# Kernel optimization log

Measured on AMD Instinct MI355X. Metric: run time of the kernel, lower is better.

The kernel has to match this reference:

```python
import jax, jax.numpy as jnp
import numpy as np

N_NODES = 50000
N_EDGES = 150000
N_GRAPHS = 1024
IN_DIM = 78
OUT_DIM = 64
HEADS = 10
HID = OUT_DIM * HEADS  # 640
NEG_SLOPE = 0.2


def _add_self_loops(edge_index, num_nodes):
    loop = jnp.arange(num_nodes, dtype=edge_index.dtype)
    src = jnp.concatenate([edge_index[0], loop])
    dst = jnp.concatenate([edge_index[1], loop])
    return src, dst


def gatv2_conv(x, edge_index, Wl, Wr, att, bias, heads, out_dim):
    # PyG GATv2Conv (share_weights=False, concat=True, add_self_loops=True),
    # inference mode so attention dropout is a no-op.
    N = x.shape[0]
    src, dst = _add_self_loops(edge_index, N)
    xl = (x @ Wl).reshape(N, heads, out_dim)  # source transform
    xr = (x @ Wr).reshape(N, heads, out_dim)  # target transform
    s = jax.nn.leaky_relu(xl[src] + xr[dst], NEG_SLOPE)      # [E,H,C]
    logits = jnp.einsum('ehc,hc->eh', s, att)                # [E,H]
    m = jax.ops.segment_max(logits, dst, num_segments=N)     # [N,H] (self-loops => no empty segs)
    ex = jnp.exp(logits - m[dst])
    den = jax.ops.segment_sum(ex, dst, num_segments=N)
    alpha = ex / den[dst]                                    # scatter-softmax over in-edges
    out = jax.ops.segment_sum(alpha[:, :, None] * xl[src], dst, num_segments=N)
    return out.reshape(N, heads * out_dim) + bias


def gcn_conv(x, edge_index, W, b):
    N = x.shape[0]
    src, dst = _add_self_loops(edge_index, N)
    deg = jax.ops.segment_sum(jnp.ones(src.shape[0], x.dtype), dst, num_segments=N)
    dinv = jax.lax.rsqrt(jnp.maximum(deg, 1.0))
    norm = dinv[src] * dinv[dst]                             # [E]
    xw = x @ W
    return jax.ops.segment_sum(norm[:, None] * xw[src], dst, num_segments=N) + b


def setup_inputs() -> dict:
    key = jax.random.key(0)
    ks = jax.random.split(key, 16)
    x = jax.random.normal(ks[0], (N_NODES, IN_DIM), dtype=jnp.float32)
    edge_index = jax.random.randint(ks[1], (2, N_EDGES), 0, N_NODES, dtype=jnp.int64)
    batch = jnp.sort(jax.random.randint(ks[2], (N_NODES,), 0, N_GRAPHS, dtype=jnp.int64))

    def glorot(k, shape, fan_in):
        return jax.random.normal(k, shape, dtype=jnp.float32) * (1.0 / np.sqrt(fan_in))

    return {
        'x': x, 'edge_index': edge_index, 'batch': batch,
        'Wl1': glorot(ks[3], (IN_DIM, HID), IN_DIM),
        'Wr1': glorot(ks[4], (IN_DIM, HID), IN_DIM),
        'a1': glorot(ks[5], (HEADS, OUT_DIM), OUT_DIM),
        'b1': jnp.zeros((HID,), jnp.float32),
        'Wl2': glorot(ks[6], (HID, HID), HID),
        'Wr2': glorot(ks[7], (HID, HID), HID),
        'a2': glorot(ks[8], (1, HID), HID),
        'b2': jnp.zeros((HID,), jnp.float32),
        'Wg': glorot(ks[9], (HID, HID), HID),
        'bg': jnp.zeros((HID,), jnp.float32),
    }


def reference(x, edge_index, batch, Wl1, Wr1, a1, b1, Wl2, Wr2, a2, b2, Wg, bg):
    # inference: feature dropout layers are identity
    h = jax.nn.elu(gatv2_conv(x, edge_index, Wl1, Wr1, a1, b1, HEADS, OUT_DIM))
    h = gatv2_conv(h, edge_index, Wl2, Wr2, a2, b2, 1, HID)
    h = gcn_conv(h, edge_index, Wg, bg)
    h = jax.nn.relu(h)
    # global max pool + global mean pool per graph
    gmax = jax.ops.segment_max(h, batch, num_segments=N_GRAPHS)
    cnt = jax.ops.segment_sum(jnp.ones((h.shape[0],), h.dtype), batch, num_segments=N_GRAPHS)
    gmean = jax.ops.segment_sum(h, batch, num_segments=N_GRAPHS) / jnp.maximum(cnt, 1.0)[:, None]
    return jnp.concatenate([gmax, gmean], axis=1)
```

## Files before the change

### kernel.cpp

```cpp
#include <hip/hip_runtime.h>
#include <hip/hip_bf16.h>
#include <cstdint>
#include <cstddef>

typedef __hip_bfloat16 bf16;

#define N_NODES  50000
#define N_EDGES  150000
#define N_GRAPHS 1024
#define IN_DIM   78
#define K1P      128
#define OUT_DIM  64
#define HEADS    10
#define HID      640
#define NEG_SLOPE 0.2f
#define SCB      ((N_NODES + 255) / 256)

static __device__ __forceinline__ float b2f(bf16 v){ return __bfloat162float(v); }
static __device__ __forceinline__ bf16  f2b(float v){ return __float2bfloat16(v); }

__device__ __forceinline__ int clampi(int v, int hi){ return v < 0 ? 0 : (v >= hi ? hi - 1 : v); }

__device__ __forceinline__ float bf2f_bits(short s){
  return __uint_as_float(((unsigned)(unsigned short)s) << 16);
}
__device__ __forceinline__ short f2bf_bits(float v){
  unsigned u = __float_as_uint(v);
  return (short)((u + 0x7fffu + ((u >> 16) & 1u)) >> 16);
}

__global__ __launch_bounds__(256) void fill_u32(unsigned* __restrict__ p, unsigned v, int n){
  int i = blockIdx.x * 256 + threadIdx.x;
  if (i < n) p[i] = v;
}

__global__ __launch_bounds__(256) void conv_x(const float* __restrict__ x, bf16* __restrict__ XB){
  int i = blockIdx.x * 256 + threadIdx.x;
  if (i >= N_NODES * K1P) return;
  int n = i / K1P, k = i - n * K1P;
  XB[i] = f2b(k < IN_DIM ? x[(size_t)n * IN_DIM + k] : 0.f);
}

__global__ __launch_bounds__(256) void conv_wT2(const float* __restrict__ W0,
                                                const float* __restrict__ W1,
                                                bf16* __restrict__ WT,
                                                int K, int N, int Kp){
  int i = blockIdx.x * 256 + threadIdx.x;
  const int per = N * Kp;
  if (i >= 2 * per) return;
  int m = i / per, r = i - m * per;
  const float* W = m == 0 ? W0 : W1;
  int n = r / Kp, k = r - n * Kp;
  WT[i] = f2b(k < K ? W[(size_t)k * N + n] : 0.f);
}

__global__ __launch_bounds__(256) void conv_wT3t(const float* __restrict__ W0,
                                                 const float* __restrict__ W1,
                                                 const float* __restrict__ W2,
                                                 bf16* __restrict__ WT){
  __shared__ float t[32][33];
  int m = blockIdx.z;
  const float* W = m == 0 ? W0 : (m == 1 ? W1 : W2);
  int n0 = blockIdx.x * 32, k0 = blockIdx.y * 32;
  int tx = threadIdx.x & 31, ty = threadIdx.x >> 5;
#pragma unroll
  for (int r = 0; r < 32; r += 8)
    t[ty + r][tx] = W[(size_t)(k0 + ty + r) * HID + n0 + tx];
  __syncthreads();
  bf16* O = WT + (size_t)m * HID * HID;
#pragma unroll
  for (int r = 0; r < 32; r += 8)
    O[(size_t)(n0 + ty + r) * HID + k0 + tx] = f2b(t[tx][ty + r]);
}

#define BM 128
#define BN 128
#define BK 64

typedef __attribute__((ext_vector_type(8))) short bf16x8;
typedef __attribute__((ext_vector_type(4))) float f32x4;

typedef const __attribute__((address_space(1))) unsigned gu32;
typedef __attribute__((address_space(3))) unsigned lu32;

__global__ __launch_bounds__(256) void mfma_gemm(const bf16* __restrict__ A,
                                                 const bf16* __restrict__ BT,
                                                 bf16* __restrict__ C0,
                                                 bf16* __restrict__ C1,
                                                 int M, int Kp, int NB){
  int d   = blockIdx.x;
  int xcd = d & 7, j = d >> 3;
  int cb  = j % NB, ri = j / NB;
  int rb  = ri * 8 + xcd;
  const int row0 = rb * BM;
  if (row0 >= M) return;
  const int col0 = cb * BN;

  __shared__ short As[BM * BK];
  __shared__ short Bs[BN * BK];
  const int tid  = threadIdx.x;
  const int lane = tid & 63;
  const int wave = tid >> 6;
  const int wr   = (wave >> 1) * 64;
  const int wc   = (wave & 1) * 64;
  const int l15  = lane & 15;
  const int quad = lane >> 4;
  const int sw   = l15 & 7;

  const bf16* aptr[4];
  const bf16* bptr[4];
  lu32* lda[4];
  lu32* ldb[4];
#pragma unroll
  for (int t = 0; t < 4; ++t){
    int ci = (t * 4 + wave) * 64 + lane;
    int r  = ci >> 3;
    int sc = (ci & 7) ^ (r & 7);
    int gr = row0 + r; if (gr >= M) gr = M - 1;
    aptr[t] = A  + (size_t)gr * Kp + sc * 8;
    bptr[t] = BT + (size_t)(col0 + r) * Kp + sc * 8;
    lda[t]  = (lu32*)(&As[(t * 4 + wave) * 512]);
    ldb[t]  = (lu32*)(&Bs[(t * 4 + wave) * 512]);
  }

  f32x4 acc[4][4];
#pragma unroll
  for (int i = 0; i < 4; ++i)
#pragma unroll
    for (int jj = 0; jj < 4; ++jj) acc[i][jj] = (f32x4){0.f, 0.f, 0.f, 0.f};

  for (int k0 = 0; k0 < Kp; k0 += BK){
#pragma unroll
    for (int t = 0; t < 4; ++t){
      __builtin_amdgcn_global_load_lds((gu32*)(aptr[t] + k0), lda[t], 16, 0, 0);
      __builtin_amdgcn_global_load_lds((gu32*)(bptr[t] + k0), ldb[t], 16, 0, 0);
    }
    __syncthreads();

#pragma unroll
    for (int ks = 0; ks < 2; ++ks){
      const int slotA = ((ks * 4 + quad) ^ sw) * 8;
      bf16x8 af[4], bfr[4];
#pragma unroll
      for (int i = 0; i < 4; ++i)
        af[i] = *(bf16x8*)(&As[(wr + i * 16 + l15) * BK + slotA]);
#pragma unroll
      for (int jj = 0; jj < 4; ++jj)
        bfr[jj] = *(bf16x8*)(&Bs[(wc + jj * 16 + l15) * BK + slotA]);
#pragma unroll
      for (int i = 0; i < 4; ++i)
#pragma unroll
        for (int jj = 0; jj < 4; ++jj)
          acc[i][jj] = __builtin_amdgcn_mfma_f32_16x16x32_bf16(af[i], bfr[jj], acc[i][jj], 0, 0, 0);
    }
    __syncthreads();
  }

  if (row0 + BM <= M){
#pragma unroll
    for (int i = 0; i < 4; ++i){
#pragma unroll
      for (int jj = 0; jj < 4; ++jj){
        int gc = col0 + wc + jj * 16 + l15;
        bf16* Cp = (gc < HID) ? C0 : C1;
        size_t cc = (gc < HID) ? gc : gc - HID;
        size_t base = (size_t)(row0 + wr + i * 16 + quad * 4) * HID + cc;
#pragma unroll
        for (int r = 0; r < 4; ++r)
          Cp[base + (size_t)r * HID] = f2b(acc[i][jj][r]);
      }
    }
  } else {
#pragma unroll
    for (int i = 0; i < 4; ++i){
#pragma unroll
      for (int jj = 0; jj < 4; ++jj){
        int gc = col0 + wc + jj * 16 + l15;
        bf16* Cp = (gc < HID) ? C0 : C1;
        int cc   = (gc < HID) ? gc : gc - HID;
#pragma unroll
        for (int r = 0; r < 4; ++r){
          int gr = row0 + wr + i * 16 + quad * 4 + r;
          if (gr < M) Cp[(size_t)gr * HID + cc] = f2b(acc[i][jj][r]);
        }
      }
    }
  }
}

__global__ __launch_bounds__(256) void count_deg(const int* __restrict__ edst, int* __restrict__ degi){
  int e = blockIdx.x * 256 + threadIdx.x;
  if (e >= N_EDGES) return;
  atomicAdd(&degi[clampi(edst[e], N_NODES)], 1);
}

__global__ __launch_bounds__(256) void scan_blk(const int* __restrict__ degi,
                                                int* __restrict__ rowp,
                                                float* __restrict__ dinv,
                                                int* __restrict__ bsum){
  __shared__ int wsum[4];
  int b = blockIdx.x, tid = threadIdx.x;
  int i = b * 256 + tid;
  int lane = tid & 63, wv = tid >> 6;
  int v = (i < N_NODES) ? degi[i] : 0;
  int incl = v;
#pragma unroll
  for (int ofs = 1; ofs < 64; ofs <<= 1){
    int t = __shfl_up(incl, ofs);
    if (lane >= ofs) incl += t;
  }
  if (lane == 63) wsum[wv] = incl;
  __syncthreads();
  int woff = 0;
#pragma unroll
  for (int w = 0; w < 4; ++w) if (w < wv) woff += wsum[w];
  if (i < N_NODES){
    rowp[i] = woff + incl - v;
    dinv[i] = rsqrtf((float)(v + 1));
  }
  if (tid == 0) bsum[b] = wsum[0] + wsum[1] + wsum[2] + wsum[3];
}

__global__ __launch_bounds__(256) void scan_top(int* __restrict__ bsum, int* __restrict__ rowp){
  __shared__ int wsum[4];
  int tid = threadIdx.x, lane = tid & 63, wv = tid >> 6;
  int v = (tid < SCB) ? bsum[tid] : 0;
  int incl = v;
#pragma unroll
  for (int ofs = 1; ofs < 64; ofs <<= 1){
    int t = __shfl_up(incl, ofs);
    if (lane >= ofs) incl += t;
  }
  if (lane == 63) wsum[wv] = incl;
  __syncthreads();
  int woff = 0;
#pragma unroll
  for (int w = 0; w < 4; ++w) if (w < wv) woff += wsum[w];
  if (tid < SCB) bsum[tid] = woff + incl - v;
  if (tid == 255) rowp[N_NODES] = woff + incl;
}

__global__ __launch_bounds__(256) void scan_add(const int* __restrict__ bsum,
                                                int* __restrict__ rowp,
                                                int* __restrict__ curs){
  int i = blockIdx.x * 256 + threadIdx.x;
  if (i >= N_NODES) return;
  int r = rowp[i] + bsum[blockIdx.x];
  rowp[i] = r; curs[i] = r;
}

__global__ __launch_bounds__(256) void bucket_edges(const int* __restrict__ esrc,
                                                    const int* __restrict__ edst,
                                                    int* __restrict__ curs,
                                                    int* __restrict__ srcg,
                                                    int* __restrict__ dstg){
  int e = blockIdx.x * 256 + threadIdx.x;
  if (e >= N_EDGES) return;
  int d = clampi(edst[e], N_NODES);
  int pos = atomicAdd(&curs[d], 1);
  srcg[pos] = clampi(esrc[e], N_NODES);
  dstg[pos] = d;
}

__global__ __launch_bounds__(256) void gat1_fused(const bf16* __restrict__ xl,
                                                  const bf16* __restrict__ xr,
                                                  const int* __restrict__ srcg,
                                                  const int* __restrict__ rowp,
                                                  const float* __restrict__ att,
                                                  const float* __restrict__ bias,
                                                  bf16* __restrict__ H){
  int n    = (blockIdx.x * 256 + threadIdx.x) >> 6;
  int lane = threadIdx.x & 63;
  if (n >= N_NODES) return;
  int r0 = rowp[n], r1 = rowp[n + 1];

  float4 aA0 = *(const float4*)(att + 8 * lane);
  float4 aA1 = *(const float4*)(att + 8 * lane + 4);
  float2 aBv = *(const float2*)(att + 512 + 2 * lane);
  float attA[8] = {aA0.x, aA0.y, aA0.z, aA0.w, aA1.x, aA1.y, aA1.z, aA1.w};
  float attB0 = aBv.x, attB1 = aBv.y;

  const bf16* xrn = xr + (size_t)n * HID;
  bf16x8 vr = *(const bf16x8*)(xrn + 8 * lane);
  unsigned ur = *(const unsigned*)(xrn + 512 + 2 * lane);
  float xrA[8];
#pragma unroll
  for (int j = 0; j < 8; ++j) xrA[j] = bf2f_bits(vr[j]);
  float xrB0 = bf2f_bits((short)(ur & 0xffff));
  float xrB1 = bf2f_bits((short)(ur >> 16));

  auto logits = [&](const float* xA, float xB0, float xB1, float& lA, float& lB){
    float pa = 0.f;
#pragma unroll
    for (int j = 0; j < 8; ++j){
      float s = xA[j] + xrA[j];
      s *= (s > 0.f) ? 1.f : NEG_SLOPE;
      pa = fmaf(attA[j], s, pa);
    }
    pa += __shfl_xor(pa, 1);
    pa += __shfl_xor(pa, 2);
    pa += __shfl_xor(pa, 4);
    lA = pa;
    float s0 = xB0 + xrB0; s0 *= (s0 > 0.f) ? 1.f : NEG_SLOPE;
    float s1 = xB1 + xrB1; s1 *= (s1 > 0.f) ? 1.f : NEG_SLOPE;
    float pb = attB0 * s0 + attB1 * s1;
    pb += __shfl_xor(pb, 1);
    pb += __shfl_xor(pb, 2);
    pb += __shfl_xor(pb, 4);
    pb += __shfl_xor(pb, 8);
    pb += __shfl_xor(pb, 16);
    lB = pb;
  };

  const bf16* xn = xl + (size_t)n * HID;
  bf16x8 v0 = *(const bf16x8*)(xn + 8 * lane);
  unsigned u0 = *(const unsigned*)(xn + 512 + 2 * lane);
  float accA[8];
  float sA[8];
#pragma unroll
  for (int j = 0; j < 8; ++j){ sA[j] = bf2f_bits(v0[j]); accA[j] = sA[j]; }
  float sB0 = bf2f_bits((short)(u0 & 0xffff));
  float sB1 = bf2f_bits((short)(u0 >> 16));
  float accB0 = sB0, accB1 = sB1;
  float mA, mB;
  logits(sA, sB0, sB1, mA, mB);
  float denA = 1.f, denB = 1.f;

  int p = r0;
  for (; p + 1 < r1; p += 2){
    int s0i = srcg[p], s1i = srcg[p + 1];
    const bf16* q0 = xl + (size_t)s0i * HID;
    const bf16* q1 = xl + (size_t)s1i * HID;
    bf16x8 w0 = *(const bf16x8*)(q0 + 8 * lane);
    unsigned t0 = *(const unsigned*)(q0 + 512 + 2 * lane);
    bf16x8 w1 = *(const bf16x8*)(q1 + 8 * lane);
    unsigned t1 = *(const unsigned*)(q1 + 512 + 2 * lane);
    float yA0[8], yA1[8];
#pragma unroll
    for (int j = 0; j < 8; ++j){ yA0[j] = bf2f_bits(w0[j]); yA1[j] = bf2f_bits(w1[j]); }
    float yB00 = bf2f_bits((short)(t0 & 0xffff)), yB01 = bf2f_bits((short)(t0 >> 16));
    float yB10 = bf2f_bits((short)(t1 & 0xffff)), yB11 = bf2f_bits((short)(t1 >> 16));
    float lA0, lB0, lA1, lB1;
    logits(yA0, yB00, yB01, lA0, lB0);
    logits(yA1, yB10, yB11, lA1, lB1);
    {
      float m2 = fmaxf(mA, fmaxf(lA0, lA1));
      float sc = __expf(mA - m2);
      float p0 = __expf(lA0 - m2), p1 = __expf(lA1 - m2);
      denA = denA * sc + p0 + p1; mA = m2;
#pragma unroll
      for (int j = 0; j < 8; ++j) accA[j] = accA[j] * sc + p0 * yA0[j] + p1 * yA1[j];
    }
    {
      float m2 = fmaxf(mB, fmaxf(lB0, lB1));
      float sc = __expf(mB - m2);
      float p0 = __expf(lB0 - m2), p1 = __expf(lB1 - m2);
      denB = denB * sc + p0 + p1; mB = m2;
      accB0 = accB0 * sc + p0 * yB00 + p1 * yB10;
      accB1 = accB1 * sc + p0 * yB01 + p1 * yB11;
    }
  }
  if (p < r1){
    int si = srcg[p];
    const bf16* q0 = xl + (size_t)si * HID;
    bf16x8 w0 = *(const bf16x8*)(q0 + 8 * lane);
    unsigned t0 = *(const unsigned*)(q0 + 512 + 2 * lane);
    float yA0[8];
#pragma unroll
    for (int j = 0; j < 8; ++j) yA0[j] = bf2f_bits(w0[j]);
    float yB00 = bf2f_bits((short)(t0 & 0xffff)), yB01 = bf2f_bits((short)(t0 >> 16));
    float lA0, lB0;
    logits(yA0, yB00, yB01, lA0, lB0);
    {
      float m2 = fmaxf(mA, lA0);
      float sc = __expf(mA - m2);
      float p0 = __expf(lA0 - m2);
      denA = denA * sc + p0; mA = m2;
#pragma unroll
      for (int j = 0; j < 8; ++j) accA[j] = accA[j] * sc + p0 * yA0[j];
    }
    {
      float m2 = fmaxf(mB, lB0);
      float sc = __expf(mB - m2);
      float p0 = __expf(lB0 - m2);
      denB = denB * sc + p0; mB = m2;
      accB0 = accB0 * sc + p0 * yB00;
      accB1 = accB1 * sc + p0 * yB01;
    }
  }

  float invA = 1.f / denA, invB = 1.f / denB;
  float4 bA0 = *(const float4*)(bias + 8 * lane);
  float4 bA1 = *(const float4*)(bias + 8 * lane + 4);
  float2 bB  = *(const float2*)(bias + 512 + 2 * lane);
  float bAa[8] = {bA0.x, bA0.y, bA0.z, bA0.w, bA1.x, bA1.y, bA1.z, bA1.w};
  bf16x8 oA;
#pragma unroll
  for (int j = 0; j < 8; ++j){
    float v = accA[j] * invA + bAa[j];
    v = v > 0.f ? v : (__expf(v) - 1.f);
    oA[j] = f2bf_bits(v);
  }
  float vb0 = accB0 * invB + bB.x; vb0 = vb0 > 0.f ? vb0 : (__expf(vb0) - 1.f);
  float vb1 = accB1 * invB + bB.y; vb1 = vb1 > 0.f ? vb1 : (__expf(vb1) - 1.f);
  bf16* hn = H + (size_t)n * HID;
  *(bf16x8*)(hn + 8 * lane) = oA;
  unsigned ob = (unsigned)(unsigned short)f2bf_bits(vb0) |
                ((unsigned)(unsigned short)f2bf_bits(vb1) << 16);
  *(unsigned*)(hn + 512 + 2 * lane) = ob;
}

__global__ __launch_bounds__(256) void gat2_fused(const bf16* __restrict__ xl,
                                                  const bf16* __restrict__ xr,
                                                  const int* __restrict__ srcg,
                                                  const int* __restrict__ rowp,
                                                  const float* __restrict__ att,
                                                  const float* __restrict__ bias,
                                                  bf16* __restrict__ H){
  int n    = (blockIdx.x * 256 + threadIdx.x) >> 6;
  int lane = threadIdx.x & 63;
  if (n >= N_NODES) return;
  int r0 = rowp[n], r1 = rowp[n + 1];

  float4 aA0 = *(const float4*)(att + 8 * lane);
  float4 aA1 = *(const float4*)(att + 8 * lane + 4);
  float2 aBv = *(const float2*)(att + 512 + 2 * lane);
  float attA[8] = {aA0.x, aA0.y, aA0.z, aA0.w, aA1.x, aA1.y, aA1.z, aA1.w};
  float attB0 = aBv.x, attB1 = aBv.y;

  const bf16* xrn = xr + (size_t)n * HID;
  bf16x8 vr = *(const bf16x8*)(xrn + 8 * lane);
  unsigned ur = *(const unsigned*)(xrn + 512 + 2 * lane);
  float xrA[8];
#pragma unroll
  for (int j = 0; j < 8; ++j) xrA[j] = bf2f_bits(vr[j]);
  float xrB0 = bf2f_bits((short)(ur & 0xffff));
  float xrB1 = bf2f_bits((short)(ur >> 16));

  auto logit1 = [&](const float* xA, float xB0, float xB1)->float{
    float s0 = xB0 + xrB0; s0 *= (s0 > 0.f) ? 1.f : NEG_SLOPE;
    float s1 = xB1 + xrB1; s1 *= (s1 > 0.f) ? 1.f : NEG_SLOPE;
    float pa = attB0 * s0 + attB1 * s1;
#pragma unroll
    for (int j = 0; j < 8; ++j){
      float s = xA[j] + xrA[j];
      s *= (s > 0.f) ? 1.f : NEG_SLOPE;
      pa = fmaf(attA[j], s, pa);
    }
    pa += __shfl_xor(pa, 1);
    pa += __shfl_xor(pa, 2);
    pa += __shfl_xor(pa, 4);
    pa += __shfl_xor(pa, 8);
    pa += __shfl_xor(pa, 16);
    pa += __shfl_xor(pa, 32);
    return pa;
  };

  const bf16* xn = xl + (size_t)n * HID;
  bf16x8 v0 = *(const bf16x8*)(xn + 8 * lane);
  unsigned u0 = *(const unsigned*)(xn + 512 + 2 * lane);
  float accA[8];
  float sA[8];
#pragma unroll
  for (int j = 0; j < 8; ++j){ sA[j] = bf2f_bits(v0[j]); accA[j] = sA[j]; }
  float sB0 = bf2f_bits((short)(u0 & 0xffff));
  float sB1 = bf2f_bits((short)(u0 >> 16));
  float accB0 = sB0, accB1 = sB1;
  float m = logit1(sA, sB0, sB1);
  float den = 1.f;

  int p = r0;
  for (; p + 1 < r1; p += 2){
    int s0i = srcg[p], s1i = srcg[p + 1];
    const bf16* q0 = xl + (size_t)s0i * HID;
    const bf16* q1 = xl + (size_t)s1i * HID;
    bf16x8 w0 = *(const bf16x8*)(q0 + 8 * lane);
    unsigned t0 = *(const unsigned*)(q0 + 512 + 2 * lane);
    bf16x8 w1 = *(const bf16x8*)(q1 + 8 * lane);
    unsigned t1 = *(const unsigned*)(q1 + 512 + 2 * lane);
    float yA0[8], yA1[8];
#pragma unroll
    for (int j = 0; j < 8; ++j){ yA0[j] = bf2f_bits(w0[j]); yA1[j] = bf2f_bits(w1[j]); }
    float yB00 = bf2f_bits((short)(t0 & 0xffff)), yB01 = bf2f_bits((short)(t0 >> 16));
    float yB10 = bf2f_bits((short)(t1 & 0xffff)), yB11 = bf2f_bits((short)(t1 >> 16));
    float l0 = logit1(yA0, yB00, yB01);
    float l1 = logit1(yA1, yB10, yB11);
    float m2 = fmaxf(m, fmaxf(l0, l1));
    float sc = __expf(m - m2);
    float p0 = __expf(l0 - m2), p1 = __expf(l1 - m2);
    den = den * sc + p0 + p1; m = m2;
#pragma unroll
    for (int j = 0; j < 8; ++j) accA[j] = accA[j] * sc + p0 * yA0[j] + p1 * yA1[j];
    accB0 = accB0 * sc + p0 * yB00 + p1 * yB10;
    accB1 = accB1 * sc + p0 * yB01 + p1 * yB11;
  }
  if (p < r1){
    int si = srcg[p];
    const bf16* q0 = xl + (size_t)si * HID;
    bf16x8 w0 = *(const bf16x8*)(q0 + 8 * lane);
    unsigned t0 = *(const unsigned*)(q0 + 512 + 2 * lane);
    float yA0[8];
#pragma unroll
    for (int j = 0; j < 8; ++j) yA0[j] = bf2f_bits(w0[j]);
    float yB00 = bf2f_bits((short)(t0 & 0xffff)), yB01 = bf2f_bits((short)(t0 >> 16));
    float l0 = logit1(yA0, yB00, yB01);
    float m2 = fmaxf(m, l0);
    float sc = __expf(m - m2);
    float p0 = __expf(l0 - m2);
    den = den * sc + p0; m = m2;
#pragma unroll
    for (int j = 0; j < 8; ++j) accA[j] = accA[j] * sc + p0 * yA0[j];
    accB0 = accB0 * sc + p0 * yB00;
    accB1 = accB1 * sc + p0 * yB01;
  }

  float inv = 1.f / den;
  float4 bA0 = *(const float4*)(bias + 8 * lane);
  float4 bA1 = *(const float4*)(bias + 8 * lane + 4);
  float2 bB  = *(const float2*)(bias + 512 + 2 * lane);
  float bAa[8] = {bA0.x, bA0.y, bA0.z, bA0.w, bA1.x, bA1.y, bA1.z, bA1.w};
  bf16x8 oA;
#pragma unroll
  for (int j = 0; j < 8; ++j) oA[j] = f2bf_bits(accA[j] * inv + bAa[j]);
  bf16* hn = H + (size_t)n * HID;
  *(bf16x8*)(hn + 8 * lane) = oA;
  unsigned ob = (unsigned)(unsigned short)f2bf_bits(accB0 * inv + bB.x) |
                ((unsigned)(unsigned short)f2bf_bits(accB1 * inv + bB.y) << 16);
  *(unsigned*)(hn + 512 + 2 * lane) = ob;
}

__global__ __launch_bounds__(256) void gcn_gather(const bf16* __restrict__ xw,
                                                  const int* __restrict__ srcg,
                                                  const int* __restrict__ rowp,
                                                  const float* __restrict__ dinv,
                                                  const float* __restrict__ bg,
                                                  bf16* __restrict__ h3){
  int n    = (blockIdx.x * 256 + threadIdx.x) >> 6;
  int lane = threadIdx.x & 63;
  if (n >= N_NODES) return;
  int r0 = rowp[n], r1 = rowp[n + 1];

  float dn = dinv[n];
  float accA[8], accB[2];
  {
    float w = dn * dn;
    const bf16* xn = xw + (size_t)n * HID;
    bf16x8 va = *(const bf16x8*)(xn + 8 * lane);
    unsigned vb = *(const unsigned*)(xn + 512 + 2 * lane);
#pragma unroll
    for (int j = 0; j < 8; ++j) accA[j] = w * bf2f_bits(va[j]);
    accB[0] = w * bf2f_bits((short)(vb & 0xffff));
    accB[1] = w * bf2f_bits((short)(vb >> 16));
  }
  int p = r0;
  for (; p + 1 < r1; p += 2){
    int s0 = srcg[p], s1 = srcg[p + 1];
    float w0 = dinv[s0] * dn, w1 = dinv[s1] * dn;
    const bf16* xs0 = xw + (size_t)s0 * HID;
    const bf16* xs1 = xw + (size_t)s1 * HID;
    bf16x8 va0 = *(const bf16x8*)(xs0 + 8 * lane);
    bf16x8 va1 = *(const bf16x8*)(xs1 + 8 * lane);
    unsigned vb0 = *(const unsigned*)(xs0 + 512 + 2 * lane);
    unsigned vb1 = *(const unsigned*)(xs1 + 512 + 2 * lane);
#pragma unroll
    for (int j = 0; j < 8; ++j) accA[j] += w0 * bf2f_bits(va0[j]) + w1 * bf2f_bits(va1[j]);
    accB[0] += w0 * bf2f_bits((short)(vb0 & 0xffff)) + w1 * bf2f_bits((short)(vb1 & 0xffff));
    accB[1] += w0 * bf2f_bits((short)(vb0 >> 16))    + w1 * bf2f_bits((short)(vb1 >> 16));
  }
  if (p < r1){
    int s = srcg[p];
    float w = dinv[s] * dn;
    const bf16* xs = xw + (size_t)s * HID;
    bf16x8 va = *(const bf16x8*)(xs + 8 * lane);
    unsigned vb = *(const unsigned*)(xs + 512 + 2 * lane);
#pragma unroll
    for (int j = 0; j < 8; ++j) accA[j] += w * bf2f_bits(va[j]);
    accB[0] += w * bf2f_bits((short)(vb & 0xffff));
    accB[1] += w * bf2f_bits((short)(vb >> 16));
  }
  float4 bA0 = *(const float4*)(bg + 8 * lane);
  float4 bA1 = *(const float4*)(bg + 8 * lane + 4);
  float2 bB  = *(const float2*)(bg + 512 + 2 * lane);
  float bAa[8] = {bA0.x, bA0.y, bA0.z, bA0.w, bA1.x, bA1.y, bA1.z, bA1.w};
  bf16x8 oA;
#pragma unroll
  for (int j = 0; j < 8; ++j) oA[j] = f2bf_bits(fmaxf(accA[j] + bAa[j], 0.f));
  bf16* hn = h3 + (size_t)n * HID;
  *(bf16x8*)(hn + 8 * lane) = oA;
  unsigned ob = (unsigned)(unsigned short)f2bf_bits(fmaxf(accB[0] + bB.x, 0.f)) |
                ((unsigned)(unsigned short)f2bf_bits(fmaxf(accB[1] + bB.y, 0.f)) << 16);
  *(unsigned*)(hn + 512 + 2 * lane) = ob;
}

__global__ __launch_bounds__(256) void graph_bounds(const int* __restrict__ batch,
                                                    int* __restrict__ gstart){
  int n = blockIdx.x * 256 + threadIdx.x;
  if (n >= N_NODES) return;
  int b = clampi(batch[n], N_GRAPHS);
  if (n == 0){
    for (int g = 0; g <= b; ++g) gstart[g] = 0;
  } else {
    int bp = clampi(batch[n - 1], N_GRAPHS);
    for (int g = bp + 1; g <= b; ++g) gstart[g] = n;
  }
  if (n == N_NODES - 1){
    for (int g = b + 1; g <= N_GRAPHS; ++g) gstart[g] = N_NODES;
  }
}

__global__ __launch_bounds__(640) void pool_graph(const bf16* __restrict__ h3,
                                                  const int* __restrict__ gstart,
                                                  float* __restrict__ out){
  int g = blockIdx.x;
  int c = threadIdx.x;
  int n0 = gstart[g], n1 = gstart[g + 1];
  float mx = 0.f, sm = 0.f;
  for (int n = n0; n < n1; ++n){
    float v = b2f(h3[(size_t)n * HID + c]);
    mx = fmaxf(mx, v); sm += v;
  }
  float mean = (n1 > n0) ? sm / (float)(n1 - n0) : 0.f;
  out[(size_t)g * 2 * HID + c]       = mx;
  out[(size_t)g * 2 * HID + HID + c] = mean;
}

extern "C" void kernel_launch(void* const* d_in, const int* in_sizes, int n_in,
                              void* d_out, int out_size, void* d_ws, size_t ws_size,
                              hipStream_t stream){
  const float* x     = (const float*)d_in[0];
  const int*   ei    = (const int*)d_in[1];
  const int*   batch = (const int*)d_in[2];
  const float* Wl1 = (const float*)d_in[3];
  const float* Wr1 = (const float*)d_in[4];
  const float* a1  = (const float*)d_in[5];
  const float* b1  = (const float*)d_in[6];
  const float* Wl2 = (const float*)d_in[7];
  const float* Wr2 = (const float*)d_in[8];
  const float* a2  = (const float*)d_in[9];
  const float* b2  = (const float*)d_in[10];
  const float* Wg  = (const float*)d_in[11];
  const float* bg  = (const float*)d_in[12];
  const int* esrc = ei;
  const int* edst = ei + N_EDGES;

  char* ws = (char*)d_ws;
  size_t off = 0;
  auto take = [&](size_t bytes)->char*{
    char* p = ws + off; off = (off + bytes + 255) & ~(size_t)255; return p;
  };
  bf16*     X1   = (bf16*)    take((size_t)N_NODES * HID * 2);
  bf16*     X2   = (bf16*)    take((size_t)N_NODES * HID * 2);
  bf16*     H    = (bf16*)    take((size_t)N_NODES * HID * 2);
  bf16*     XB   = (bf16*)    take((size_t)N_NODES * K1P * 2);
  bf16*     WT1l = (bf16*)    take((size_t)HID * K1P * 2);
  bf16*     WT1r = (bf16*)    take((size_t)HID * K1P * 2);
  bf16*     WT2l = (bf16*)    take((size_t)HID * HID * 2);
  bf16*     WT2r = (bf16*)    take((size_t)HID * HID * 2);
  bf16*     WTg  = (bf16*)    take((size_t)HID * HID * 2);
  int*      DEGI = (int*)     take((size_t)N_NODES * 4);
  int*      ROWP = (int*)     take((size_t)(N_NODES + 1) * 4);
  int*      CURS = (int*)     take((size_t)N_NODES * 4);
  int*      SRCG = (int*)     take((size_t)N_EDGES * 4);
  int*      DSTG = (int*)     take((size_t)N_EDGES * 4);
  float*    DINV = (float*)   take((size_t)N_NODES * 4);
  int*      GST  = (int*)     take((size_t)(N_GRAPHS + 1) * 4);
  int*      BSUM = (int*)     take((size_t)SCB * 4);
  (void)WT1r; (void)WT2r; (void)DSTG;

  dim3 blk(256);
  auto fill = [&](void* p, unsigned v, int n){
    fill_u32<<<dim3((n + 255) / 256), blk, 0, stream>>>((unsigned*)p, v, n);
  };
  const int MB8     = ((N_NODES + BM - 1) / BM + 7) / 8;
  const int nblocks = (N_NODES * 64 + 255) / 256;
  const int reblk   = (N_EDGES + 255) / 256;

  conv_x<<<(N_NODES * K1P + 255) / 256, blk, 0, stream>>>(x, XB);
  conv_wT2<<<(2 * HID * K1P + 255) / 256, blk, 0, stream>>>(Wl1, Wr1, WT1l, IN_DIM, HID, K1P);
  conv_wT3t<<<dim3(HID / 32, HID / 32, 3), blk, 0, stream>>>(Wl2, Wr2, Wg, WT2l);
  fill(DEGI, 0u, N_NODES);
  count_deg<<<reblk, blk, 0, stream>>>(edst, DEGI);
  scan_blk<<<dim3(SCB), blk, 0, stream>>>(DEGI, ROWP, DINV, BSUM);
  scan_top<<<dim3(1), blk, 0, stream>>>(BSUM, ROWP);
  scan_add<<<dim3(SCB), blk, 0, stream>>>(BSUM, ROWP, CURS);
  bucket_edges<<<reblk, blk, 0, stream>>>(esrc, edst, CURS, SRCG, DSTG);
  graph_bounds<<<(N_NODES + 255) / 256, blk, 0, stream>>>(batch, GST);

  mfma_gemm<<<dim3(8 * MB8 * 10), blk, 0, stream>>>(XB, WT1l, X1, X2, N_NODES, K1P, 10);
  gat1_fused<<<nblocks, blk, 0, stream>>>(X1, X2, SRCG, ROWP, a1, b1, H);

  mfma_gemm<<<dim3(8 * MB8 * 10), blk, 0, stream>>>(H, WT2l, X1, X2, N_NODES, HID, 10);
  gat2_fused<<<nblocks, blk, 0, stream>>>(X1, X2, SRCG, ROWP, a2, b2, H);

  mfma_gemm<<<dim3(8 * MB8 * 5), blk, 0, stream>>>(H, WTg, X1, X1, N_NODES, HID, 5);
  gcn_gather<<<nblocks, blk, 0, stream>>>(X1, SRCG, ROWP, DINV, bg, X2);
  pool_graph<<<dim3(N_GRAPHS), dim3(640), 0, stream>>>(X2, GST, (float*)d_out);
}
```

Baseline: 511.5 us.

## Add 256x256-tile 512-thread MFMA GEMM with 4-stage LDS pipeline for layer 2/GCN

Adds a second GEMM kernel using 256x256 output tiles, 8 waves per block, and a 4-deep global_load_lds ring buffer with three stages in flight. It is used for the GATv2 layer-2 and GCN projections instead of the original smaller-tile kernel. The goal is more reuse per loaded tile and better latency hiding on these K=640 GEMMs. In exchange it uses 128KB of LDS and many accumulator registers per block, which lowers occupancy. The GCN GEMM (640 columns) also pads to three 256-wide column tiles, wasting part of the last one.

```diff
diff --git a/kernel.cpp b/kernel.cpp
--- a/kernel.cpp
+++ b/kernel.cpp
@@ -182,6 +182,157 @@
         for (int r = 0; r < 4; ++r){
           int gr = row0 + wr + i * 16 + quad * 4 + r;
           if (gr < M) Cp[(size_t)gr * HID + cc] = f2b(acc[i][jj][r]);
+        }
+      }
+    }
+  }
+}
+
+#define BM2 256
+#define BN2 256
+
+__global__ __launch_bounds__(512) void mfma_gemm2(const bf16* __restrict__ A,
+                                                  const bf16* __restrict__ BT,
+                                                  bf16* __restrict__ C0,
+                                                  bf16* __restrict__ C1,
+                                                  int M, int Ntot, int Kp, int NB){
+  int d   = blockIdx.x;
+  int xcd = d & 7, j = d >> 3;
+  int cb  = j % NB, ri = j / NB;
+  int rb  = ri * 8 + xcd;
+  const int row0 = rb * BM2;
+  if (row0 >= M) return;
+  const int col0 = cb * BN2;
+
+  __shared__ short LDS[4 * 16384];
+  const int tid  = threadIdx.x;
+  const int lane = tid & 63;
+  const int wave = tid >> 6;
+  const int l15  = lane & 15;
+  const int quad = lane >> 4;
+  const int wr   = (wave >> 2) * 128;
+  const int wc   = (wave & 3) * 64;
+
+  const int KT = Kp / 32;
+
+  const int rs0 = wave * 16 + (lane >> 2);
+  const int rs1 = rs0 + 128;
+  const int sl  = lane & 3;
+  const int c0  = sl ^ ((rs0 >> 1) & 3);
+  const int c1  = sl ^ ((rs1 >> 1) & 3);
+  int grA0 = row0 + rs0; if (grA0 >= M)    grA0 = M - 1;
+  int grA1 = row0 + rs1; if (grA1 >= M)    grA1 = M - 1;
+  int gcB0 = col0 + rs0; if (gcB0 >= Ntot) gcB0 = Ntot - 1;
+  int gcB1 = col0 + rs1; if (gcB1 >= Ntot) gcB1 = Ntot - 1;
+  const bf16* gA0 = A  + (size_t)grA0 * Kp + c0 * 8;
+  const bf16* gA1 = A  + (size_t)grA1 * Kp + c1 * 8;
+  const bf16* gB0 = BT + (size_t)gcB0 * Kp + c0 * 8;
+  const bf16* gB1 = BT + (size_t)gcB1 * Kp + c1 * 8;
+  const int ldsA0 = wave * 512;
+  const int ldsA1 = 4096 + wave * 512;
+  const int ldsB0 = 8192 + wave * 512;
+  const int ldsB1 = 12288 + wave * 512;
+
+  auto stage = [&](int t){
+    const int bb = (t & 3) * 16384;
+    const int k0 = t * 32;
+    __builtin_amdgcn_global_load_lds((gu32*)(gA0 + k0), (lu32*)(&LDS[bb + ldsA0]), 16, 0, 0);
+    __builtin_amdgcn_global_load_lds((gu32*)(gA1 + k0), (lu32*)(&LDS[bb + ldsA1]), 16, 0, 0);
+    __builtin_amdgcn_global_load_lds((gu32*)(gB0 + k0), (lu32*)(&LDS[bb + ldsB0]), 16, 0, 0);
+    __builtin_amdgcn_global_load_lds((gu32*)(gB1 + k0), (lu32*)(&LDS[bb + ldsB1]), 16, 0, 0);
+  };
+
+  int aoff[8], boff[4];
+#pragma unroll
+  for (int i = 0; i < 8; ++i){
+    int r = wr + i * 16 + l15;
+    aoff[i] = r * 32 + (quad ^ ((r >> 1) & 3)) * 8;
+  }
+#pragma unroll
+  for (int jj = 0; jj < 4; ++jj){
+    int r = wc + jj * 16 + l15;
+    boff[jj] = 8192 + r * 32 + (quad ^ ((r >> 1) & 3)) * 8;
+  }
+
+  f32x4 acc[8][4];
+#pragma unroll
+  for (int i = 0; i < 8; ++i)
+#pragma unroll
+    for (int jj = 0; jj < 4; ++jj) acc[i][jj] = (f32x4){0.f, 0.f, 0.f, 0.f};
+
+  stage(0); stage(1); stage(2);
+  asm volatile("s_waitcnt vmcnt(8)" ::: "memory");
+  __builtin_amdgcn_s_barrier();
+  __builtin_amdgcn_sched_barrier(0);
+
+  for (int k = 0; k < KT; ++k){
+    const int bb = (k & 3) * 16384;
+    if (k + 3 < KT) stage(k + 3);
+
+    bf16x8 bfr[4];
+#pragma unroll
+    for (int jj = 0; jj < 4; ++jj) bfr[jj] = *(bf16x8*)(&LDS[bb + boff[jj]]);
+    bf16x8 af[4];
+#pragma unroll
+    for (int i = 0; i < 4; ++i) af[i] = *(bf16x8*)(&LDS[bb + aoff[i]]);
+    __builtin_amdgcn_s_setprio(1);
+#pragma unroll
+    for (int i = 0; i < 4; ++i)
+#pragma unroll
+      for (int jj = 0; jj < 4; ++jj)
+        acc[i][jj] = __builtin_amdgcn_mfma_f32_16x16x32_bf16(af[i], bfr[jj], acc[i][jj], 0, 0, 0);
+    __builtin_amdgcn_s_setprio(0);
+
+    bf16x8 ag[4];
+#pragma unroll
+    for (int i = 0; i < 4; ++i) ag[i] = *(bf16x8*)(&LDS[bb + aoff[4 + i]]);
+    __builtin_amdgcn_s_setprio(1);
+#pragma unroll
+    for (int i = 0; i < 4; ++i)
+#pragma unroll
+      for (int jj = 0; jj < 4; ++jj)
+        acc[4 + i][jj] = __builtin_amdgcn_mfma_f32_16x16x32_bf16(ag[i], bfr[jj], acc[4 + i][jj], 0, 0, 0);
+    __builtin_amdgcn_s_setprio(0);
+
+    if (k < KT - 1){
+      if (k < KT - 3)       { asm volatile("s_waitcnt vmcnt(8)" ::: "memory"); }
+      else if (k == KT - 3) { asm volatile("s_waitcnt vmcnt(4)" ::: "memory"); }
+      else                  { asm volatile("s_waitcnt vmcnt(0)" ::: "memory"); }
+      __builtin_amdgcn_s_barrier();
+      __builtin_amdgcn_sched_barrier(0);
+    }
+  }
+
+  if (row0 + BM2 <= M){
+#pragma unroll
+    for (int i = 0; i < 8; ++i){
+#pragma unroll
+      for (int jj = 0; jj < 4; ++jj){
+        int gc = col0 + wc + jj * 16 + l15;
+        if (gc < Ntot){
+          bf16* Cp = (gc < HID) ? C0 : C1;
+          size_t cc = (gc < HID) ? gc : gc - HID;
+          size_t base = (size_t)(row0 + wr + i * 16 + quad * 4) * HID + cc;
+#pragma unroll
+          for (int r = 0; r < 4; ++r)
+            Cp[base + (size_t)r * HID] = f2b(acc[i][jj][r]);
+        }
+      }
+    }
+  } else {
+#pragma unroll
+    for (int i = 0; i < 8; ++i){
+#pragma unroll
+      for (int jj = 0; jj < 4; ++jj){
+        int gc = col0 + wc + jj * 16 + l15;
+        if (gc < Ntot){
+          bf16* Cp = (gc < HID) ? C0 : C1;
+          int cc   = (gc < HID) ? gc : gc - HID;
+#pragma unroll
+          for (int r = 0; r < 4; ++r){
+            int gr = row0 + wr + i * 16 + quad * 4 + r;
+            if (gr < M) Cp[(size_t)gr * HID + cc] = f2b(acc[i][jj][r]);
+          }
         }
       }
     }
@@ -672,6 +823,7 @@
     fill_u32<<<dim3((n + 255) / 256), blk, 0, stream>>>((unsigned*)p, v, n);
   };
   const int MB8     = ((N_NODES + BM - 1) / BM + 7) / 8;
+  const int MB28    = ((N_NODES + BM2 - 1) / BM2 + 7) / 8;
   const int nblocks = (N_NODES * 64 + 255) / 256;
   const int reblk   = (N_EDGES + 255) / 256;
 
@@ -689,10 +841,10 @@
   mfma_gemm<<<dim3(8 * MB8 * 10), blk, 0, stream>>>(XB, WT1l, X1, X2, N_NODES, K1P, 10);
   gat1_fused<<<nblocks, blk, 0, stream>>>(X1, X2, SRCG, ROWP, a1, b1, H);
 
-  mfma_gemm<<<dim3(8 * MB8 * 10), blk, 0, stream>>>(H, WT2l, X1, X2, N_NODES, HID, 10);
+  mfma_gemm2<<<dim3(8 * MB28 * 5), dim3(512), 0, stream>>>(H, WT2l, X1, X2, N_NODES, 2 * HID, HID, 5);
   gat2_fused<<<nblocks, blk, 0, stream>>>(X1, X2, SRCG, ROWP, a2, b2, H);
 
-  mfma_gemm<<<dim3(8 * MB8 * 5), blk, 0, stream>>>(H, WTg, X1, X1, N_NODES, HID, 5);
+  mfma_gemm2<<<dim3(8 * MB28 * 3), dim3(512), 0, stream>>>(H, WTg, X1, X1, N_NODES, HID, HID, 3);
   gcn_gather<<<nblocks, blk, 0, stream>>>(X1, SRCG, ROWP, DINV, bg, X2);
   pool_graph<<<dim3(N_GRAPHS), dim3(640), 0, stream>>>(X2, GST, (float*)d_out);
 }
```

Result: slower. 523.0 us (+2.2%).
